# Performance work log

Measured on AMD Instinct MI355X. Metric: run time of the kernel, lower is better.

## Reference

```python
import jax, jax.numpy as jnp
import numpy as np

B, D = 8192, 1024
C, K = 1000, 8
EPS = 1e-15


def setup_inputs() -> dict:
    key = jax.random.key(0)
    k1, k2 = jax.random.split(key)
    # points inside the unit Poincare ball (c=1): scale so E||x|| ~ 0.64 < 1
    x = jax.random.normal(k1, (B, D), dtype=jnp.float32) * 0.02
    weight_v = jax.random.normal(k2, (C, K, D), dtype=jnp.float32)
    weight_g = jnp.ones((C,), dtype=jnp.float32)
    gamma = jnp.ones((), dtype=jnp.float32)
    return {"x": x, "weight_v": weight_v, "weight_g": weight_g, "gamma": gamma}


def reference(x, weight_v, weight_g, gamma):
    # PoincareBall curvature c = 1.0 -> rc = sqrt(c) = 1.0
    rc = jnp.asarray(1.0, dtype=x.dtype)
    # unit prototype directions: [C, K, D]
    z_norm = jnp.maximum(jnp.linalg.norm(weight_v, axis=-1, keepdims=True), EPS)
    z_unit = weight_v / z_norm
    rcx = rc * x                                   # [B, D]
    cx2 = jnp.sum(rcx * rcx, axis=-1, keepdims=True)  # [B, 1]
    inner = jnp.einsum('bd,ckd->bck', rcx, z_unit)    # [B, C, K]
    drcr = 2.0 * rc * gamma
    num = 2.0 * inner * jnp.cosh(drcr) - (1.0 + cx2[:, :, None]) * jnp.sinh(drcr)
    den = jnp.maximum(1.0 - cx2, EPS)              # [B, 1]
    logits_ck = (2.0 * weight_g[None, :, None] / rc) * jnp.arcsinh(num / den[:, :, None])
    logits = jax.nn.logsumexp(logits_ck, axis=-1)  # [B, C]
    return logits
```

## Files before the change

### kernel.cpp

```cpp
#include <hip/hip_runtime.h>
#include <hip/hip_bf16.h>
#include <stdint.h>

#define B_ROWS 8192
#define D_DIM  1024
#define C_CLS  1000
#define K_PROT 8
#define N_REAL 8000
#define N_PAD  8064
#define BM 128
#define BN 128
#define BKT 64

typedef __attribute__((ext_vector_type(8))) short  short8;
typedef __attribute__((ext_vector_type(4))) float  f32x4;


__device__ __forceinline__ ushort f2bf(float f) {
    union { float f; uint32_t u; } v; v.f = f;
    uint32_t u = v.u;
    return (ushort)((u + 0x7fffu + ((u >> 16) & 1u)) >> 16);
}

typedef __attribute__((address_space(1))) void gv_t;
typedef __attribute__((address_space(3))) void lv_t;

__device__ __forceinline__ void gload_lds16(const void* g, void* l) {
    __builtin_amdgcn_global_load_lds((gv_t*)g, (lv_t*)l, 16, 0, 0);
}

__device__ __forceinline__ float waveReduceSum(float s) {
    #pragma unroll
    for (int m = 32; m >= 1; m >>= 1) s += __shfl_xor(s, m);
    return s;
}


__global__ __launch_bounds__(256) void prep_z(const float* __restrict__ wv,
                                              ushort* __restrict__ zb) {
    const int P = blockIdx.x;
    const int t = threadIdx.x;
    __shared__ float red[4];

    const int bn  = P >> 7;
    const int p7  = P & 127;
    const int wc  = (p7 >> 6) & 1;
    const int ni  = (p7 >> 4) & 3;
    const int c   = p7 & 15;
    const int cls = bn * 16 + wc * 8 + (c & 7);
    const int k   = ni + ((c >> 3) << 2);

    if (cls >= C_CLS) {
        ((ushort4*)(zb + (size_t)P * D_DIM))[t] = make_ushort4(0, 0, 0, 0);
        return;
    }
    const int n = cls * K_PROT + k;
    const float4 v = ((const float4*)(wv + (size_t)n * D_DIM))[t];
    float s = v.x*v.x + v.y*v.y + v.z*v.z + v.w*v.w;
    s = waveReduceSum(s);
    if ((t & 63) == 0) red[t >> 6] = s;
    __syncthreads();
    const float n2 = red[0] + red[1] + red[2] + red[3];
    const float rn = 1.0f / fmaxf(sqrtf(n2), 1e-15f);
    ushort4 o;
    o.x = f2bf(v.x * rn); o.y = f2bf(v.y * rn);
    o.z = f2bf(v.z * rn); o.w = f2bf(v.w * rn);
    ((ushort4*)(zb + (size_t)P * D_DIM))[t] = o;
}


__global__ __launch_bounds__(256) void prep_x(const float* __restrict__ x,
                                              ushort* __restrict__ xb,
                                              float* __restrict__ cx2) {
    const int b = blockIdx.x;
    const int t = threadIdx.x;
    __shared__ float red[4];

    const float4 v = ((const float4*)(x + (size_t)b * D_DIM))[t];
    ushort4 o;
    o.x = f2bf(v.x); o.y = f2bf(v.y); o.z = f2bf(v.z); o.w = f2bf(v.w);
    ((ushort4*)(xb + (size_t)b * D_DIM))[t] = o;

    float s = v.x*v.x + v.y*v.y + v.z*v.z + v.w*v.w;
    s = waveReduceSum(s);
    if ((t & 63) == 0) red[t >> 6] = s;
    __syncthreads();
    if (t == 0) cx2[b] = red[0] + red[1] + red[2] + red[3];
}


__global__ __launch_bounds__(256, 2) void gemm_epi(
        const ushort* __restrict__ A,
        const ushort* __restrict__ Bz,
        const float*  __restrict__ cx2g,
        const float*  __restrict__ wgl,
        const float*  __restrict__ gamma_p,
        float*        __restrict__ out)
{
    __shared__ __attribute__((aligned(16))) ushort sA[BM * BKT];
    __shared__ __attribute__((aligned(16))) ushort sB[BN * BKT];

    const int tid  = threadIdx.x;
    const int lane = tid & 63;
    const int w    = tid >> 6;
    const int wr   = w >> 1;
    const int wc   = w & 1;

    const int bm = blockIdx.x & 63;
    const int bn = blockIdx.x >> 6;
    const int m0 = bm * BM;
    const int n0 = bn * BN;

    const int stRow = w * 32 + (lane >> 3);
    const int stCol = ((lane & 7) ^ ((lane >> 3) & 7)) * 8;

    const int swz0 = ((      (lane >> 4) * 16) ^ ((lane & 7) << 4));
    const int swz1 = ((64 + ((lane >> 4) * 16)) ^ ((lane & 7) << 4));
    const char* sAb = (const char*)sA + (wr * 64 + (lane & 15)) * 128;
    const char* sBb = (const char*)sB + (wc * 64 + (lane & 15)) * 128;

    f32x4 acc[4][4];
    #pragma unroll
    for (int mi = 0; mi < 4; ++mi)
        #pragma unroll
        for (int ni = 0; ni < 4; ++ni)
            acc[mi][ni] = (f32x4)(0.0f);

    for (int t = 0; t < D_DIM / BKT; ++t) {
        const int k0 = t * BKT;
        #pragma unroll
        for (int i = 0; i < 4; ++i) {
            gload_lds16(A  + (size_t)(m0 + stRow + i * 8) * D_DIM + k0 + stCol,
                        &sA[(w * 32 + i * 8) * BKT]);
            gload_lds16(Bz + (size_t)(n0 + stRow + i * 8) * D_DIM + k0 + stCol,
                        &sB[(w * 32 + i * 8) * BKT]);
        }
        __syncthreads();

        #pragma unroll
        for (int kk = 0; kk < 2; ++kk) {
            const int swzk = kk ? swz1 : swz0;
            short8 a[4], b[4];
            #pragma unroll
            for (int mi = 0; mi < 4; ++mi)
                a[mi] = *(const short8*)(sAb + mi * 16 * 128 + swzk);
            #pragma unroll
            for (int ni = 0; ni < 4; ++ni)
                b[ni] = *(const short8*)(sBb + ni * 16 * 128 + swzk);
            #pragma unroll
            for (int mi = 0; mi < 4; ++mi)
                #pragma unroll
                for (int ni = 0; ni < 4; ++ni)
                    acc[mi][ni] = __builtin_amdgcn_mfma_f32_16x16x32_bf16(
                        a[mi], b[ni], acc[mi][ni], 0, 0, 0);
        }
        __syncthreads();
    }

    float* scx = (float*)sA;
    if (tid < BM) scx[tid] = cx2g[m0 + tid];
    __syncthreads();

    const float gam = gamma_p[0];
    const float ex  = expf(2.0f * gam);
    const float ch2 = ex + 1.0f / ex;
    const float sh  = 0.5f * (ex - 1.0f / ex);

    const int  cls = (bn << 4) + (wc << 3) + (lane & 7);
    const bool wrt = ((lane & 8) == 0) && (cls < C_CLS);
    const float w2 = (cls < C_CLS) ? 2.0f * wgl[cls] : 0.0f;

    #pragma unroll
    for (int mi = 0; mi < 4; ++mi) {
        #pragma unroll
        for (int r = 0; r < 4; ++r) {
            const int mloc = wr * 64 + mi * 16 + ((lane >> 4) << 2) + r;
            const float c2   = scx[mloc];
            const float rden = 1.0f / fmaxf(1.0f - c2, 1e-15f);
            const float tc   = ch2 * rden;
            const float tp   = (1.0f + c2) * sh * rden;
            float bk[4];
            #pragma unroll
            for (int ni = 0; ni < 4; ++ni) {
                const float t = fmaf(acc[mi][ni][r], tc, -tp);
                const float u = fmaxf(t + __fsqrt_rn(fmaf(t, t, 1.0f)), 1e-20f);
                bk[ni] = w2 * __logf(u);
            }
            float mx = fmaxf(fmaxf(bk[0], bk[1]), fmaxf(bk[2], bk[3]));
            mx = fmaxf(mx, __shfl_xor(mx, 8));
            float s = __expf(bk[0] - mx) + __expf(bk[1] - mx)
                    + __expf(bk[2] - mx) + __expf(bk[3] - mx);
            s += __shfl_xor(s, 8);
            if (wrt)
                out[(size_t)(m0 + mloc) * C_CLS + cls] = mx + __logf(s);
        }
    }
}


extern "C" void kernel_launch(void* const* d_in, const int* in_sizes, int n_in,
                              void* d_out, int out_size, void* d_ws, size_t ws_size,
                              hipStream_t stream) {
    const float* x     = (const float*)d_in[0];
    const float* wv    = (const float*)d_in[1];
    const float* wg    = (const float*)d_in[2];
    const float* gamma = (const float*)d_in[3];
    float* out = (float*)d_out;

    char* ws = (char*)d_ws;
    ushort* xb  = (ushort*)ws;
    ushort* zb  = (ushort*)(ws + (size_t)B_ROWS * D_DIM * 2);
    float*  cx2 = (float*)(ws + (size_t)B_ROWS * D_DIM * 2
                              + (size_t)N_PAD * D_DIM * 2);

    prep_z<<<N_PAD, 256, 0, stream>>>(wv, zb);
    prep_x<<<B_ROWS, 256, 0, stream>>>(x, xb, cx2);
    gemm_epi<<<64 * 63, 256, 0, stream>>>(xb, zb, cx2, wg, gamma, out);
}
```

Before: 174.4 us.

## Restructure GEMM into 256x256 tiles with 4-stage async LDS pipeline

```diff
diff --git a/kernel.cpp b/kernel.cpp
--- a/kernel.cpp
+++ b/kernel.cpp
@@ -6,11 +6,11 @@
 #define D_DIM  1024
 #define C_CLS  1000
 #define K_PROT 8
-#define N_REAL 8000
-#define N_PAD  8064
-#define BM 128
-#define BN 128
-#define BKT 64
+#define N_PAD  8192
+#define BK     32
+#define NT     32
+#define SLOTB  32768
+#define BOFF   16384
 
 typedef __attribute__((ext_vector_type(8))) short  short8;
 typedef __attribute__((ext_vector_type(4))) float  f32x4;
@@ -42,13 +42,11 @@
     const int t = threadIdx.x;
     __shared__ float red[4];
 
-    const int bn  = P >> 7;
-    const int p7  = P & 127;
-    const int wc  = (p7 >> 6) & 1;
-    const int ni  = (p7 >> 4) & 3;
-    const int c   = p7 & 15;
-    const int cls = bn * 16 + wc * 8 + (c & 7);
-    const int k   = ni + ((c >> 3) << 2);
+    const int gpan = P >> 6;
+    const int ni   = (P >> 4) & 3;
+    const int cc   = P & 15;
+    const int cls  = gpan * 8 + (cc & 7);
+    const int k    = ni + ((cc >> 3) << 2);
 
     if (cls >= C_CLS) {
         ((ushort4*)(zb + (size_t)P * D_DIM))[t] = make_ushort4(0, 0, 0, 0);
@@ -89,7 +87,7 @@
 }
 
 
-__global__ __launch_bounds__(256, 2) void gemm_epi(
+__global__ __launch_bounds__(512, 2) void gemm_epi(
         const ushort* __restrict__ A,
         const ushort* __restrict__ Bz,
         const float*  __restrict__ cx2g,
@@ -97,68 +95,103 @@
         const float*  __restrict__ gamma_p,
         float*        __restrict__ out)
 {
-    __shared__ __attribute__((aligned(16))) ushort sA[BM * BKT];
-    __shared__ __attribute__((aligned(16))) ushort sB[BN * BKT];
+    __shared__ __attribute__((aligned(128))) char lds[4 * SLOTB];
 
     const int tid  = threadIdx.x;
     const int lane = tid & 63;
-    const int w    = tid >> 6;
-    const int wr   = w >> 1;
-    const int wc   = w & 1;
-
-    const int bm = blockIdx.x & 63;
-    const int bn = blockIdx.x >> 6;
-    const int m0 = bm * BM;
-    const int n0 = bn * BN;
-
-    const int stRow = w * 32 + (lane >> 3);
-    const int stCol = ((lane & 7) ^ ((lane >> 3) & 7)) * 8;
-
-    const int swz0 = ((      (lane >> 4) * 16) ^ ((lane & 7) << 4));
-    const int swz1 = ((64 + ((lane >> 4) * 16)) ^ ((lane & 7) << 4));
-    const char* sAb = (const char*)sA + (wr * 64 + (lane & 15)) * 128;
-    const char* sBb = (const char*)sB + (wc * 64 + (lane & 15)) * 128;
-
-    f32x4 acc[4][4];
+    const int wid  = tid >> 6;
+    const int wm   = wid >> 2;
+    const int wn   = wid & 3;
+
+    const int bid = blockIdx.x;
+    const int bm  = (bid >> 3) & 31;
+    const int bn  = 4 * (bid & 7) + (bid >> 8);
+    const int m0  = bm * 256;
+    const int n0  = bn * 256;
+
+    const int rSt = tid >> 2;
+    const int cSt = (tid & 3) ^ ((tid >> 3) & 3);
+    const ushort* aS0 = A  + (size_t)(m0 + rSt) * D_DIM + cSt * 8;
+    const ushort* aS1 = aS0 + (size_t)128 * D_DIM;
+    const ushort* bS0 = Bz + (size_t)(n0 + rSt) * D_DIM + cSt * 8;
+    const ushort* bS1 = bS0 + (size_t)128 * D_DIM;
+    const int ldsW = wid * 1024;
+
+    const int swz = ((lane >> 4) ^ ((lane & 6) >> 1)) * 16;
+    const int aOf = (wm * 128 + (lane & 15)) * 64 + swz;
+    const int bOf = (wn * 64  + (lane & 15)) * 64 + swz;
+
+#define STAGE_A(ct) do { char* sb_ = lds + ((ct) & 3) * SLOTB; \
+    const int kq_ = (ct) * BK; \
+    gload_lds16(aS0 + kq_, sb_ + ldsW); \
+    gload_lds16(aS1 + kq_, sb_ + 8192 + ldsW); } while (0)
+#define STAGE_B(ct) do { char* sb_ = lds + ((ct) & 3) * SLOTB + BOFF; \
+    const int kq_ = (ct) * BK; \
+    gload_lds16(bS0 + kq_, sb_ + ldsW); \
+    gload_lds16(bS1 + kq_, sb_ + 8192 + ldsW); } while (0)
+#define FENCE() asm volatile("" ::: "memory")
+
+    f32x4 acc[8][4];
     #pragma unroll
-    for (int mi = 0; mi < 4; ++mi)
+    for (int i = 0; i < 8; ++i)
+        #pragma unroll
+        for (int j = 0; j < 4; ++j) acc[i][j] = (f32x4)(0.0f);
+
+    STAGE_A(0); STAGE_B(0); STAGE_A(1); STAGE_B(1); STAGE_A(2); STAGE_B(2);
+    asm volatile("s_waitcnt vmcnt(8)" ::: "memory");
+    __builtin_amdgcn_s_barrier();
+    FENCE();
+
+    for (int c = 0; c < NT; ++c) {
+        const char* As = lds + (c & 3) * SLOTB;
+        const char* Bs = As + BOFF;
+        short8 a[4], b[4];
+        #pragma unroll
+        for (int mi = 0; mi < 4; ++mi)
+            a[mi] = *(const short8*)(As + aOf + mi * 1024);
         #pragma unroll
         for (int ni = 0; ni < 4; ++ni)
-            acc[mi][ni] = (f32x4)(0.0f);
-
-    for (int t = 0; t < D_DIM / BKT; ++t) {
-        const int k0 = t * BKT;
-        #pragma unroll
-        for (int i = 0; i < 4; ++i) {
-            gload_lds16(A  + (size_t)(m0 + stRow + i * 8) * D_DIM + k0 + stCol,
-                        &sA[(w * 32 + i * 8) * BKT]);
-            gload_lds16(Bz + (size_t)(n0 + stRow + i * 8) * D_DIM + k0 + stCol,
-                        &sB[(w * 32 + i * 8) * BKT]);
-        }
-        __syncthreads();
-
-        #pragma unroll
-        for (int kk = 0; kk < 2; ++kk) {
-            const int swzk = kk ? swz1 : swz0;
-            short8 a[4], b[4];
-            #pragma unroll
-            for (int mi = 0; mi < 4; ++mi)
-                a[mi] = *(const short8*)(sAb + mi * 16 * 128 + swzk);
+            b[ni] = *(const short8*)(Bs + bOf + ni * 1024);
+        if (c <= NT - 4) STAGE_A(c + 3);
+        FENCE();
+        __builtin_amdgcn_s_barrier();
+        FENCE();
+        __builtin_amdgcn_s_setprio(1);
+        #pragma unroll
+        for (int mi = 0; mi < 4; ++mi)
             #pragma unroll
             for (int ni = 0; ni < 4; ++ni)
-                b[ni] = *(const short8*)(sBb + ni * 16 * 128 + swzk);
+                acc[mi][ni] = __builtin_amdgcn_mfma_f32_16x16x32_bf16(
+                    a[mi], b[ni], acc[mi][ni], 0, 0, 0);
+        __builtin_amdgcn_s_setprio(0);
+        FENCE();
+        __builtin_amdgcn_s_barrier();
+        FENCE();
+        #pragma unroll
+        for (int mi = 0; mi < 4; ++mi)
+            a[mi] = *(const short8*)(As + aOf + (mi + 4) * 1024);
+        if (c <= NT - 4) STAGE_B(c + 3);
+        FENCE();
+        __builtin_amdgcn_s_barrier();
+        FENCE();
+        __builtin_amdgcn_s_setprio(1);
+        #pragma unroll
+        for (int mi = 0; mi < 4; ++mi)
             #pragma unroll
-            for (int mi = 0; mi < 4; ++mi)
-                #pragma unroll
-                for (int ni = 0; ni < 4; ++ni)
-                    acc[mi][ni] = __builtin_amdgcn_mfma_f32_16x16x32_bf16(
-                        a[mi], b[ni], acc[mi][ni], 0, 0, 0);
-        }
-        __syncthreads();
+            for (int ni = 0; ni < 4; ++ni)
+                acc[mi + 4][ni] = __builtin_amdgcn_mfma_f32_16x16x32_bf16(
+                    a[mi], b[ni], acc[mi + 4][ni], 0, 0, 0);
+        __builtin_amdgcn_s_setprio(0);
+        if (c <= NT - 4)      asm volatile("s_waitcnt vmcnt(8)" ::: "memory");
+        else if (c == NT - 3) asm volatile("s_waitcnt vmcnt(4)" ::: "memory");
+        else if (c == NT - 2) asm volatile("s_waitcnt vmcnt(0)" ::: "memory");
+        __builtin_amdgcn_s_barrier();
+        FENCE();
     }
 
-    float* scx = (float*)sA;
-    if (tid < BM) scx[tid] = cx2g[m0 + tid];
+    __syncthreads();
+    float* scx = (float*)lds;
+    if (tid < 256) scx[tid] = cx2g[m0 + tid];
     __syncthreads();
 
     const float gam = gamma_p[0];
@@ -166,15 +199,16 @@
     const float ch2 = ex + 1.0f / ex;
     const float sh  = 0.5f * (ex - 1.0f / ex);
 
-    const int  cls = (bn << 4) + (wc << 3) + (lane & 7);
+    const int  pan = (n0 >> 6) + wn;
+    const int  cls = pan * 8 + (lane & 7);
     const bool wrt = ((lane & 8) == 0) && (cls < C_CLS);
     const float w2 = (cls < C_CLS) ? 2.0f * wgl[cls] : 0.0f;
 
     #pragma unroll
-    for (int mi = 0; mi < 4; ++mi) {
+    for (int mi = 0; mi < 8; ++mi) {
         #pragma unroll
         for (int r = 0; r < 4; ++r) {
-            const int mloc = wr * 64 + mi * 16 + ((lane >> 4) << 2) + r;
+            const int mloc = wm * 128 + mi * 16 + ((lane >> 4) << 2) + r;
             const float c2   = scx[mloc];
             const float rden = 1.0f / fmaxf(1.0f - c2, 1e-15f);
             const float tc   = ch2 * rden;
@@ -195,6 +229,9 @@
                 out[(size_t)(m0 + mloc) * C_CLS + cls] = mx + __logf(s);
         }
     }
+#undef STAGE_A
+#undef STAGE_B
+#undef FENCE
 }
 
 
@@ -215,5 +252,5 @@
 
     prep_z<<<N_PAD, 256, 0, stream>>>(wv, zb);
     prep_x<<<B_ROWS, 256, 0, stream>>>(x, xb, cx2);
-    gemm_epi<<<64 * 63, 256, 0, stream>>>(xb, zb, cx2, wg, gamma, out);
-}
+    gemm_epi<<<1024, 512, 0, stream>>>(xb, zb, cx2, wg, gamma, out);
+}
```

Result: slower. 215.4 us (+23.5%).
